# Kernel tuning notes

Measured on AMD Instinct MI355X. Metric: run time of the kernel, lower is better.

## Reference

```python
import jax, jax.numpy as jnp
import numpy as np
from jax import lax

START_IDX = 1  # ludwig strings_utils.START_IDX


def setup_inputs() -> dict:
    key = jax.random.key(0)
    ks = jax.random.split(key, 8)
    B, T, H, V = 32, 128, 512, 32000
    scale = 0.05
    return {
        "encoder_output_state": jax.random.normal(ks[0], (B, H), jnp.float32),
        "target": jax.random.randint(ks[1], (B, T), 0, V, jnp.int64),
        "E": jax.random.normal(ks[2], (V, H), jnp.float32) * scale,
        "W_ih": jax.random.normal(ks[3], (4 * H, H), jnp.float32) * scale,
        "W_hh": jax.random.normal(ks[4], (4 * H, H), jnp.float32) * scale,
        "b_ih": jax.random.normal(ks[5], (4 * H,), jnp.float32) * scale,
        "b_hh": jax.random.normal(ks[6], (4 * H,), jnp.float32) * scale,
        "b_out": jax.random.normal(ks[7], (V,), jnp.float32) * scale,
    }


def reference(encoder_output_state, target, E, W_ih, W_hh, b_ih, b_hh, b_out):
    # Teacher-forcing decode: step 0 consumes START_IDX, step t consumes target[:, t-1].
    B, T = target.shape
    start = jnp.full((B, 1), START_IDX, dtype=target.dtype)
    inputs = jnp.concatenate([start, target[:, :-1]], axis=1)  # [B, T]

    def step(carry, tok):
        h, c = carry  # each [B, H]
        x = E[tok]  # embedding lookup [B, H]
        # PyTorch LSTM gate layout: [i, f, g, o]
        gates = x @ W_ih.T + b_ih + h @ W_hh.T + b_hh  # [B, 4H]
        i, f, g, o = jnp.split(gates, 4, axis=-1)
        i = jax.nn.sigmoid(i)
        f = jax.nn.sigmoid(f)
        g = jnp.tanh(g)
        o = jax.nn.sigmoid(o)
        c = f * c + i * g
        h = o * jnp.tanh(c)
        logits = h @ E.T + b_out  # tied output projection [B, V]
        return (h, c), logits

    h0 = encoder_output_state
    c0 = encoder_output_state  # original sets cell_state = hidden = encoder state
    _, logits = lax.scan(step, (h0, c0), inputs.T)  # logits [T, B, V]
    return jnp.transpose(logits, (1, 0, 2))  # [B, T, V]
```

## Files before the change

kernel.cpp:

```cpp
#include <hip/hip_runtime.h>
#include <hip/hip_bf16.h>
#include <cstdint>
#include <cstddef>

typedef __bf16 bf16_t;
typedef __bf16 bf16x8 __attribute__((ext_vector_type(8)));
typedef __bf16 bf16x4 __attribute__((ext_vector_type(4)));
typedef float  f32x4  __attribute__((ext_vector_type(4)));

#define B_  32
#define T_  128
#define H_  512
#define V_  32000
#define G4_ 2048
#define NB_ 64
#define HBUF_ (B_ * H_)


__global__ void convert_f32_bf16(const float* __restrict__ src, bf16_t* __restrict__ dst, int n4) {
  int i = blockIdx.x * blockDim.x + threadIdx.x;
  int stride = gridDim.x * blockDim.x;
  for (; i < n4; i += stride) {
    float4 v = ((const float4*)src)[i];
    bf16x4 o = { (bf16_t)v.x, (bf16_t)v.y, (bf16_t)v.z, (bf16_t)v.w };
    ((bf16x4*)dst)[i] = o;
  }
}

__global__ void gather_embed(const float* __restrict__ E, const int* __restrict__ target,
                             bf16_t* __restrict__ Xemb) {
  int n = blockIdx.x;
  int b = n >> 7, t = n & 127;
  int tok = (t == 0) ? 1 : target[b * T_ + t - 1];
  const float4* src = (const float4*)(E + (size_t)tok * H_);
  bf16x4* dst = (bf16x4*)(Xemb + (size_t)n * H_);
  int k = threadIdx.x;
  float4 v = src[k];
  bf16x4 o = { (bf16_t)v.x, (bf16_t)v.y, (bf16_t)v.z, (bf16_t)v.w };
  dst[k] = o;
}

__global__ void init_misc(const float* __restrict__ b_ih, const float* __restrict__ b_hh,
                          float* __restrict__ bsum, unsigned* __restrict__ slots,
                          unsigned* __restrict__ go) {
  int i = blockIdx.x * blockDim.x + threadIdx.x;
  if (i < G4_) bsum[i] = b_ih[i] + b_hh[i];
  if (i < NB_) slots[i] = 0;
  if (i == 0) *go = 0;
}

__global__ __launch_bounds__(256)
void gemm_bt(const bf16_t* __restrict__ A, const bf16_t* __restrict__ Bm,
             const float* __restrict__ bias, float* __restrict__ C, int N) {
  __shared__ bf16_t As[128 * 64];
  __shared__ bf16_t Bs[128 * 64];
  const int tid  = threadIdx.x;
  const int tn   = blockIdx.x;
  const int tm   = blockIdx.y;
  const int lane = tid & 63, wid = tid >> 6;
  const int wm = (wid >> 1) * 64, wn = (wid & 1) * 64;
  const size_t K = 512;

  f32x4 acc[4][4] = {};

  for (int k0 = 0; k0 < 512; k0 += 64) {
    #pragma unroll
    for (int r = 0; r < 4; ++r) {
      int c   = r * 256 + tid;
      int row = c >> 3, kc = c & 7;
      const bf16_t* ga = A  + ((size_t)(tm * 128 + row)) * K + (size_t)k0 + kc * 8;
      const bf16_t* gb = Bm + ((size_t)(tn * 128 + row)) * K + (size_t)k0 + kc * 8;
      __builtin_amdgcn_global_load_lds((__attribute__((address_space(1))) void*)ga,
                                       (__attribute__((address_space(3))) void*)(As + c * 8),
                                       16, 0, 0);
      __builtin_amdgcn_global_load_lds((__attribute__((address_space(1))) void*)gb,
                                       (__attribute__((address_space(3))) void*)(Bs + c * 8),
                                       16, 0, 0);
    }
    __syncthreads();

    #pragma unroll
    for (int k32 = 0; k32 < 64; k32 += 32) {
      bf16x8 af[4], bfr[4];
      const int kk = k32 + (lane >> 4) * 8;
      #pragma unroll
      for (int i = 0; i < 4; ++i) {
        int ra = wm + i * 16 + (lane & 15);
        af[i]  = *(const bf16x8*)(As + ra * 64 + kk);
        int rb = wn + i * 16 + (lane & 15);
        bfr[i] = *(const bf16x8*)(Bs + rb * 64 + kk);
      }
      #pragma unroll
      for (int i = 0; i < 4; ++i)
        #pragma unroll
        for (int j = 0; j < 4; ++j)
          acc[i][j] = __builtin_amdgcn_mfma_f32_16x16x32_bf16(af[i], bfr[j], acc[i][j], 0, 0, 0);
    }
    __syncthreads();
  }

  const int m0 = tm * 128 + wm + (lane >> 4) * 4;
  const int n0 = tn * 128 + wn + (lane & 15);
  #pragma unroll
  for (int i = 0; i < 4; ++i) {
    #pragma unroll
    for (int j = 0; j < 4; ++j) {
      int nn = n0 + j * 16;
      float bv = bias ? bias[nn] : 0.f;
      #pragma unroll
      for (int r = 0; r < 4; ++r) {
        int mm = m0 + i * 16 + r;
        C[(size_t)mm * N + nn] = acc[i][j][r] + bv;
      }
    }
  }
}


static __device__ __forceinline__ unsigned bperm_lo16(unsigned u0, unsigned u1) {
  return __builtin_amdgcn_perm(u1, u0, 0x05040100u);
}
static __device__ __forceinline__ unsigned bperm_hi16(unsigned u0, unsigned u1) {
  return __builtin_amdgcn_perm(u1, u0, 0x07060302u);
}
static __device__ __forceinline__ unsigned pack_hl(float h, bf16_t& hh_out) {
  bf16_t hh = (bf16_t)h;
  bf16_t hl = (bf16_t)(h - (float)hh);
  hh_out = hh;
  union { bf16_t b; unsigned short u; } a, b2;
  a.b = hh; b2.b = hl;
  return (unsigned)a.u | ((unsigned)b2.u << 16);
}

__device__ __forceinline__ void grid_bar(unsigned* slots, unsigned* go, unsigned tok) {
  __syncthreads();
  if (threadIdx.x == 0)
    __hip_atomic_store(&slots[blockIdx.x], tok, __ATOMIC_RELEASE, __HIP_MEMORY_SCOPE_AGENT);
  if (blockIdx.x == 0) {
    if (threadIdx.x < 64) {
      for (;;) {
        unsigned v = __hip_atomic_load(&slots[threadIdx.x], __ATOMIC_ACQUIRE,
                                       __HIP_MEMORY_SCOPE_AGENT);
        if (__all((int)(v >= tok))) break;
        __builtin_amdgcn_s_sleep(1);
      }
      if (threadIdx.x == 0)
        __hip_atomic_store(go, tok, __ATOMIC_RELEASE, __HIP_MEMORY_SCOPE_AGENT);
    }
  } else if (threadIdx.x == 0) {
    while (__hip_atomic_load(go, __ATOMIC_ACQUIRE, __HIP_MEMORY_SCOPE_AGENT) < tok)
      __builtin_amdgcn_s_sleep(1);
  }
  __syncthreads();
}

__global__ __launch_bounds__(256, 1)
void lstm_persist(const float* __restrict__ Xg, const float* __restrict__ Whh,
                  const float* __restrict__ enc, unsigned* __restrict__ h_pk,
                  bf16_t* __restrict__ Hall,
                  unsigned* __restrict__ slots, unsigned* __restrict__ go) {
  __shared__ __attribute__((aligned(16))) float gsh[2][32][36];

  const int tid  = threadIdx.x;
  const int lane = tid & 63;
  const int w    = tid >> 6;
  const int mt   = w & 1;
  const int kh   = w >> 1;
  const int m0   = blockIdx.x * 8;
  const int rl   = lane & 15;
  const int kc   = (lane >> 4) * 8;

  bf16x8 whi[2][8], wlo[2][8];
  #pragma unroll
  for (int nt = 0; nt < 2; ++nt) {
    const int r  = nt * 16 + rl;
    const int g  = r & 3, ml = r >> 2;
    const float* wrow = Whh + (size_t)(g * H_ + m0 + ml) * H_ + kh * 256 + kc;
    #pragma unroll
    for (int i = 0; i < 8; ++i) {
      float4 f0 = *(const float4*)(wrow + i * 32);
      float4 f1 = *(const float4*)(wrow + i * 32 + 4);
      bf16x8 hi8, lo8;
      hi8[0] = (bf16_t)f0.x; lo8[0] = (bf16_t)(f0.x - (float)hi8[0]);
      hi8[1] = (bf16_t)f0.y; lo8[1] = (bf16_t)(f0.y - (float)hi8[1]);
      hi8[2] = (bf16_t)f0.z; lo8[2] = (bf16_t)(f0.z - (float)hi8[2]);
      hi8[3] = (bf16_t)f0.w; lo8[3] = (bf16_t)(f0.w - (float)hi8[3]);
      hi8[4] = (bf16_t)f1.x; lo8[4] = (bf16_t)(f1.x - (float)hi8[4]);
      hi8[5] = (bf16_t)f1.y; lo8[5] = (bf16_t)(f1.y - (float)hi8[5]);
      hi8[6] = (bf16_t)f1.z; lo8[6] = (bf16_t)(f1.z - (float)hi8[6]);
      hi8[7] = (bf16_t)f1.w; lo8[7] = (bf16_t)(f1.w - (float)hi8[7]);
      whi[nt][i] = hi8; wlo[nt][i] = lo8;
    }
  }

  const int pb  = tid >> 3;
  const int pml = tid & 7;
  const int pm  = m0 + pml;
  float c = enc[pb * H_ + pm];
  {
    bf16_t dummy;
    unsigned pkv = pack_hl(c, dummy);
    __hip_atomic_store(&h_pk[pb * H_ + pm], pkv, __ATOMIC_RELAXED, __HIP_MEMORY_SCOPE_AGENT);
  }
  grid_bar(slots, go, 1u);

  const unsigned abase = (unsigned)(mt * 16 + rl) * H_ + (unsigned)(kh * 256 + kc);

  for (int t = 0; t < T_; ++t) {
    const unsigned rboff = (unsigned)(t & 1) * HBUF_;
    const unsigned wboff = (unsigned)((t + 1) & 1) * HBUF_;

    const float* xg = Xg + ((size_t)pb * T_ + t) * G4_ + pm;
    float x0 = xg[0], x1 = xg[512], x2 = xg[1024], x3 = xg[1536];

    unsigned long long pkv[8][4];
    #pragma unroll
    for (int i = 0; i < 8; ++i) {
      const unsigned long long* hp =
          (const unsigned long long*)(h_pk + rboff + abase + i * 32);
      #pragma unroll
      for (int q = 0; q < 4; ++q)
        pkv[i][q] = __hip_atomic_load(hp + q, __ATOMIC_RELAXED, __HIP_MEMORY_SCOPE_AGENT);
    }

    f32x4 acc[2][3] = {};
    #pragma unroll
    for (int i = 0; i < 8; ++i) {
      unsigned u0 = (unsigned)pkv[i][0], u1 = (unsigned)(pkv[i][0] >> 32);
      unsigned u2 = (unsigned)pkv[i][1], u3 = (unsigned)(pkv[i][1] >> 32);
      unsigned u4 = (unsigned)pkv[i][2], u5 = (unsigned)(pkv[i][2] >> 32);
      unsigned u6 = (unsigned)pkv[i][3], u7 = (unsigned)(pkv[i][3] >> 32);
      union { unsigned u[4]; bf16x8 v; } ah, al;
      ah.u[0] = bperm_lo16(u0, u1); ah.u[1] = bperm_lo16(u2, u3);
      ah.u[2] = bperm_lo16(u4, u5); ah.u[3] = bperm_lo16(u6, u7);
      al.u[0] = bperm_hi16(u0, u1); al.u[1] = bperm_hi16(u2, u3);
      al.u[2] = bperm_hi16(u4, u5); al.u[3] = bperm_hi16(u6, u7);
      acc[0][0] = __builtin_amdgcn_mfma_f32_16x16x32_bf16(ah.v, whi[0][i], acc[0][0], 0, 0, 0);
      acc[1][0] = __builtin_amdgcn_mfma_f32_16x16x32_bf16(ah.v, whi[1][i], acc[1][0], 0, 0, 0);
      acc[0][1] = __builtin_amdgcn_mfma_f32_16x16x32_bf16(ah.v, wlo[0][i], acc[0][1], 0, 0, 0);
      acc[1][1] = __builtin_amdgcn_mfma_f32_16x16x32_bf16(ah.v, wlo[1][i], acc[1][1], 0, 0, 0);
      acc[0][2] = __builtin_amdgcn_mfma_f32_16x16x32_bf16(al.v, whi[0][i], acc[0][2], 0, 0, 0);
      acc[1][2] = __builtin_amdgcn_mfma_f32_16x16x32_bf16(al.v, whi[1][i], acc[1][2], 0, 0, 0);
    }

    #pragma unroll
    for (int nt = 0; nt < 2; ++nt) {
      f32x4 s = acc[nt][0] + acc[nt][1] + acc[nt][2];
      #pragma unroll
      for (int q = 0; q < 4; ++q)
        gsh[kh][mt * 16 + (lane >> 4) * 4 + q][nt * 16 + rl] = s[q];
    }
    __syncthreads();

    float4 v0 = *(const float4*)&gsh[0][pb][pml * 4];
    float4 v1 = *(const float4*)&gsh[1][pb][pml * 4];
    float gi = v0.x + v1.x + x0;
    float gf = v0.y + v1.y + x1;
    float gg = v0.z + v1.z + x2;
    float gv = v0.w + v1.w + x3;
    float si = 1.f / (1.f + expf(-gi));
    float sf = 1.f / (1.f + expf(-gf));
    float tg = tanhf(gg);
    float so = 1.f / (1.f + expf(-gv));
    c = sf * c + si * tg;
    float h = so * tanhf(c);
    bf16_t hh;
    unsigned pko = pack_hl(h, hh);
    Hall[((size_t)pb * T_ + t) * H_ + pm] = hh;
    __hip_atomic_store(&h_pk[wboff + pb * H_ + pm], pko, __ATOMIC_RELAXED,
                       __HIP_MEMORY_SCOPE_AGENT);

    if (t < T_ - 1) grid_bar(slots, go, (unsigned)(t + 2));
  }
}


extern "C" void kernel_launch(void* const* d_in, const int* in_sizes, int n_in,
                              void* d_out, int out_size, void* d_ws, size_t ws_size,
                              hipStream_t stream) {
  const float* enc    = (const float*)d_in[0];
  const int*   target = (const int*)  d_in[1];
  const float* E      = (const float*)d_in[2];
  const float* W_ih   = (const float*)d_in[3];
  const float* W_hh   = (const float*)d_in[4];
  const float* b_ih   = (const float*)d_in[5];
  const float* b_hh   = (const float*)d_in[6];
  const float* b_out  = (const float*)d_in[7];
  float* out = (float*)d_out;

  char* p = (char*)d_ws;
  bf16_t*  E_bf   = (bf16_t*)p;   p += (size_t)V_ * H_ * 2;
  bf16_t*  Wih_bf = (bf16_t*)p;   p += (size_t)G4_ * H_ * 2;
  bf16_t*  Xemb   = (bf16_t*)p;   p += (size_t)B_ * T_ * H_ * 2;
  bf16_t*  Hall   = (bf16_t*)p;   p += (size_t)B_ * T_ * H_ * 2;
  float*   Xg     = (float*)p;    p += (size_t)B_ * T_ * G4_ * 4;
  float*   bsum   = (float*)p;    p += (size_t)G4_ * 4;
  unsigned* h_pk  = (unsigned*)p; p += (size_t)2 * HBUF_ * 4;
  unsigned* slots = (unsigned*)p; p += NB_ * 4;
  unsigned* go    = (unsigned*)p; p += 256;

  convert_f32_bf16<<<2048, 256, 0, stream>>>(E, E_bf, V_ * H_ / 4);
  convert_f32_bf16<<<256, 256, 0, stream>>>(W_ih, Wih_bf, G4_ * H_ / 4);
  gather_embed<<<B_ * T_, 128, 0, stream>>>(E, target, Xemb);
  init_misc<<<8, 256, 0, stream>>>(b_ih, b_hh, bsum, slots, go);

  dim3 g1(G4_ / 128, (B_ * T_) / 128);
  gemm_bt<<<g1, 256, 0, stream>>>(Xemb, Wih_bf, bsum, Xg, G4_);

  lstm_persist<<<NB_, 256, 0, stream>>>(Xg, W_hh, enc, h_pk, Hall, slots, go);

  dim3 g2(V_ / 128, (B_ * T_) / 128);
  gemm_bt<<<g2, 256, 0, stream>>>(Hall, E_bf, b_out, out, V_);
}
```

Measured before the change: 1.929 ms.

## Replace centralized grid barrier with per-wave dependency flags in LSTM recurrence

```diff
diff --git a/kernel.cpp b/kernel.cpp
--- a/kernel.cpp
+++ b/kernel.cpp
@@ -14,6 +14,7 @@
 #define V_  32000
 #define G4_ 2048
 #define NB_ 64
+#define NSLOT_ 256
 #define HBUF_ (B_ * H_)
 
 
@@ -41,12 +42,10 @@
 }
 
 __global__ void init_misc(const float* __restrict__ b_ih, const float* __restrict__ b_hh,
-                          float* __restrict__ bsum, unsigned* __restrict__ slots,
-                          unsigned* __restrict__ go) {
+                          float* __restrict__ bsum, unsigned* __restrict__ slots) {
   int i = blockIdx.x * blockDim.x + threadIdx.x;
   if (i < G4_) bsum[i] = b_ih[i] + b_hh[i];
-  if (i < NB_) slots[i] = 0;
-  if (i == 0) *go = 0;
+  if (i < NSLOT_) slots[i] = 0;
 }
 
 __global__ __launch_bounds__(256)
@@ -132,34 +131,11 @@
   return (unsigned)a.u | ((unsigned)b2.u << 16);
 }
 
-__device__ __forceinline__ void grid_bar(unsigned* slots, unsigned* go, unsigned tok) {
-  __syncthreads();
-  if (threadIdx.x == 0)
-    __hip_atomic_store(&slots[blockIdx.x], tok, __ATOMIC_RELEASE, __HIP_MEMORY_SCOPE_AGENT);
-  if (blockIdx.x == 0) {
-    if (threadIdx.x < 64) {
-      for (;;) {
-        unsigned v = __hip_atomic_load(&slots[threadIdx.x], __ATOMIC_ACQUIRE,
-                                       __HIP_MEMORY_SCOPE_AGENT);
-        if (__all((int)(v >= tok))) break;
-        __builtin_amdgcn_s_sleep(1);
-      }
-      if (threadIdx.x == 0)
-        __hip_atomic_store(go, tok, __ATOMIC_RELEASE, __HIP_MEMORY_SCOPE_AGENT);
-    }
-  } else if (threadIdx.x == 0) {
-    while (__hip_atomic_load(go, __ATOMIC_ACQUIRE, __HIP_MEMORY_SCOPE_AGENT) < tok)
-      __builtin_amdgcn_s_sleep(1);
-  }
-  __syncthreads();
-}
-
 __global__ __launch_bounds__(256, 1)
 void lstm_persist(const float* __restrict__ Xg, const float* __restrict__ Whh,
                   const float* __restrict__ enc, unsigned* __restrict__ h_pk,
-                  bf16_t* __restrict__ Hall,
-                  unsigned* __restrict__ slots, unsigned* __restrict__ go) {
-  __shared__ __attribute__((aligned(16))) float gsh[2][32][36];
+                  bf16_t* __restrict__ Hall, unsigned* __restrict__ slots) {
+  __shared__ __attribute__((aligned(16))) float gsh[2][2][32][36];
 
   const int tid  = threadIdx.x;
   const int lane = tid & 63;
@@ -196,15 +172,18 @@
   const int pb  = tid >> 3;
   const int pml = tid & 7;
   const int pm  = m0 + pml;
+  const int myslot = blockIdx.x * 4 + w;
   float c = enc[pb * H_ + pm];
   {
     bf16_t dummy;
-    unsigned pkv = pack_hl(c, dummy);
-    __hip_atomic_store(&h_pk[pb * H_ + pm], pkv, __ATOMIC_RELAXED, __HIP_MEMORY_SCOPE_AGENT);
-  }
-  grid_bar(slots, go, 1u);
+    unsigned pkv0 = pack_hl(c, dummy);
+    __hip_atomic_store(&h_pk[pb * H_ + pm], pkv0, __ATOMIC_RELAXED, __HIP_MEMORY_SCOPE_AGENT);
+  }
+  if (lane == 0)
+    __hip_atomic_store(&slots[myslot], 1u, __ATOMIC_RELEASE, __HIP_MEMORY_SCOPE_AGENT);
 
   const unsigned abase = (unsigned)(mt * 16 + rl) * H_ + (unsigned)(kh * 256 + kc);
+  const int pidx = 128 * kh + 4 * (lane >> 1) + 2 * mt + (lane & 1);
 
   for (int t = 0; t < T_; ++t) {
     const unsigned rboff = (unsigned)(t & 1) * HBUF_;
@@ -212,6 +191,15 @@
 
     const float* xg = Xg + ((size_t)pb * T_ + t) * G4_ + pm;
     float x0 = xg[0], x1 = xg[512], x2 = xg[1024], x3 = xg[1536];
+
+    {
+      const unsigned tok = (unsigned)(t + 1);
+      for (;;) {
+        unsigned v = __hip_atomic_load(&slots[pidx], __ATOMIC_ACQUIRE,
+                                       __HIP_MEMORY_SCOPE_AGENT);
+        if (__all((int)(v >= tok))) break;
+      }
+    }
 
     unsigned long long pkv[8][4];
     #pragma unroll
@@ -248,12 +236,12 @@
       f32x4 s = acc[nt][0] + acc[nt][1] + acc[nt][2];
       #pragma unroll
       for (int q = 0; q < 4; ++q)
-        gsh[kh][mt * 16 + (lane >> 4) * 4 + q][nt * 16 + rl] = s[q];
+        gsh[t & 1][kh][mt * 16 + (lane >> 4) * 4 + q][nt * 16 + rl] = s[q];
     }
     __syncthreads();
 
-    float4 v0 = *(const float4*)&gsh[0][pb][pml * 4];
-    float4 v1 = *(const float4*)&gsh[1][pb][pml * 4];
+    float4 v0 = *(const float4*)&gsh[t & 1][0][pb][pml * 4];
+    float4 v1 = *(const float4*)&gsh[t & 1][1][pb][pml * 4];
     float gi = v0.x + v1.x + x0;
     float gf = v0.y + v1.y + x1;
     float gg = v0.z + v1.z + x2;
@@ -266,11 +254,12 @@
     float h = so * tanhf(c);
     bf16_t hh;
     unsigned pko = pack_hl(h, hh);
-    Hall[((size_t)pb * T_ + t) * H_ + pm] = hh;
     __hip_atomic_store(&h_pk[wboff + pb * H_ + pm], pko, __ATOMIC_RELAXED,
                        __HIP_MEMORY_SCOPE_AGENT);
-
-    if (t < T_ - 1) grid_bar(slots, go, (unsigned)(t + 2));
+    if (t < T_ - 1 && lane == 0)
+      __hip_atomic_store(&slots[myslot], (unsigned)(t + 2), __ATOMIC_RELEASE,
+                         __HIP_MEMORY_SCOPE_AGENT);
+    Hall[((size_t)pb * T_ + t) * H_ + pm] = hh;
   }
 }
 
@@ -296,18 +285,17 @@
   float*   Xg     = (float*)p;    p += (size_t)B_ * T_ * G4_ * 4;
   float*   bsum   = (float*)p;    p += (size_t)G4_ * 4;
   unsigned* h_pk  = (unsigned*)p; p += (size_t)2 * HBUF_ * 4;
-  unsigned* slots = (unsigned*)p; p += NB_ * 4;
-  unsigned* go    = (unsigned*)p; p += 256;
+  unsigned* slots = (unsigned*)p; p += NSLOT_ * 4;
 
   convert_f32_bf16<<<2048, 256, 0, stream>>>(E, E_bf, V_ * H_ / 4);
   convert_f32_bf16<<<256, 256, 0, stream>>>(W_ih, Wih_bf, G4_ * H_ / 4);
   gather_embed<<<B_ * T_, 128, 0, stream>>>(E, target, Xemb);
-  init_misc<<<8, 256, 0, stream>>>(b_ih, b_hh, bsum, slots, go);
+  init_misc<<<8, 256, 0, stream>>>(b_ih, b_hh, bsum, slots);
 
   dim3 g1(G4_ / 128, (B_ * T_) / 128);
   gemm_bt<<<g1, 256, 0, stream>>>(Xemb, Wih_bf, bsum, Xg, G4_);
 
-  lstm_persist<<<NB_, 256, 0, stream>>>(Xg, W_hh, enc, h_pk, Hall, slots, go);
+  lstm_persist<<<NB_, 256, 0, stream>>>(Xg, W_hh, enc, h_pk, Hall, slots);
 
   dim3 g2(V_ / 128, (B_ * T_) / 128);
   gemm_bt<<<g2, 256, 0, stream>>>(Hall, E_bf, b_out, out, V_);
```

After: 2.444 ms. 26.7% more time.
